# Performance work log

Measured on AMD Instinct MI355X. Metric: run time of the kernel, lower is better.

Reference implementation:

```python
import jax, jax.numpy as jnp
import numpy as np

W_DIM = 512
C_IN = 512
C_OUT = 512
K = 3
EPS = 1e-6
STYLE_SCALE = 1.0 / np.sqrt(W_DIM)              # EqualizedWeight scale for (out,in)
CONV_SCALE = 1.0 / np.sqrt(C_IN * K * K)        # EqualizedWeight scale for (out,in,k,k)


def setup_inputs() -> dict:
    key = jax.random.key(0)
    ks = jax.random.split(key, 6)
    B, H, W = 16, 64, 64
    return {
        "x": jax.random.normal(ks[0], (B, C_IN, H, W), dtype=jnp.float32),
        "w": jax.random.normal(ks[1], (B, W_DIM), dtype=jnp.float32),
        "style_weight": jax.random.normal(ks[2], (C_IN, W_DIM), dtype=jnp.float32),
        "style_bias": jnp.zeros((C_IN,), dtype=jnp.float32),
        "conv_weight": jax.random.normal(ks[3], (C_OUT, C_IN, K, K), dtype=jnp.float32),
        "noise_weight": jax.random.normal(ks[4], (1, C_OUT, 1, 1), dtype=jnp.float32),
        "bias": jnp.zeros((C_OUT,), dtype=jnp.float32),
        "noise": jax.random.normal(ks[5], (B, 1, H, W), dtype=jnp.float32),
    }


def reference(x, w, style_weight, style_bias, conv_weight, noise_weight, bias, noise):
    B, _, H, Wd = x.shape
    # to_style: equalized linear  [B, C_IN]
    s = w @ (style_weight * STYLE_SCALE).T + style_bias
    # modulate: [B, C_OUT, C_IN, K, K]
    wts = (conv_weight * CONV_SCALE)[None] * s[:, None, :, None, None]
    # demodulate
    sigma = jax.lax.rsqrt(jnp.sum(wts * wts, axis=(2, 3, 4)) + EPS)  # [B, C_OUT]
    wts = wts * sigma[:, :, None, None, None]
    # grouped conv with groups = batch
    x_r = x.reshape(1, B * C_IN, H, Wd)
    w_r = wts.reshape(B * C_OUT, C_IN, K, K)
    y = jax.lax.conv_general_dilated(
        x_r, w_r, window_strides=(1, 1), padding=[(1, 1), (1, 1)],
        dimension_numbers=("NCHW", "OIHW", "NCHW"), feature_group_count=B,
    ).reshape(B, C_OUT, H, Wd)
    # noise injection + bias + leaky relu(0.2)
    y = y + noise_weight * noise + bias[None, :, None, None]
    return jax.nn.leaky_relu(y, negative_slope=0.2)
```

## Files before the change

kernel.cpp:

```cpp
#include <hip/hip_runtime.h>


typedef __attribute__((ext_vector_type(8))) short short8;
typedef __attribute__((ext_vector_type(4))) float f32x4;

#define STYLE_SCALE 0.044194173824159216f
#define CONV_SCALE  0.014731391274719742f
#define CS2         (1.0f/4608.0f)

static __device__ __forceinline__ unsigned short f2bf(float x) {
    union { float f; unsigned int u; } a; a.f = x;
    unsigned int r = a.u + 0x7fffu + ((a.u >> 16) & 1u);
    return (unsigned short)(r >> 16);
}

static __device__ __forceinline__ void gl_lds16(const void* g, void* l) {
    __builtin_amdgcn_global_load_lds(
        (const __attribute__((address_space(1))) unsigned int*)g,
        (__attribute__((address_space(3))) unsigned int*)l, 16, 0, 0);
}

__global__ void k_style(const float* __restrict__ w, const float* __restrict__ sw,
                        const float* __restrict__ sb, float* __restrict__ s) {
    int b = blockIdx.y, j0 = blockIdx.x * 64, t = threadIdx.x;
    __shared__ float wl[512];
    __shared__ float part[256];
    wl[t] = w[b*512 + t]; wl[t+256] = w[b*512 + t + 256];
    __syncthreads();
    int jl = t & 63, seg = t >> 6;
    const float4* row = (const float4*)(sw + (size_t)(j0 + jl)*512) + seg*32;
    const float*  wv  = wl + seg*128;
    float acc = 0.f;
#pragma unroll 4
    for (int k = 0; k < 32; ++k) {
        float4 v = row[k];
        acc += v.x*wv[4*k] + v.y*wv[4*k+1] + v.z*wv[4*k+2] + v.w*wv[4*k+3];
    }
    part[t] = acc;
    __syncthreads();
    if (t < 64)
        s[b*512 + j0 + t] = (part[t] + part[t+64] + part[t+128] + part[t+192])
                            * STYLE_SCALE + sb[j0 + t];
}

__global__ void k_wprep(const float* __restrict__ cw, float* __restrict__ csq,
                        unsigned short* __restrict__ cwt) {
    int o = blockIdx.x, t = threadIdx.x;
    __shared__ float row[4608];
    const float4* src = (const float4*)(cw + (size_t)o*4608);
    for (int i = t; i < 1152; i += 256) ((float4*)row)[i] = src[i];
    __syncthreads();
#pragma unroll
    for (int it = 0; it < 2; ++it) {
        int i = t + it*256;
        float a = 0.f;
#pragma unroll
        for (int k = 0; k < 9; ++k) { float v = row[i*9 + k]; a += v*v; }
        csq[(size_t)o*512 + i] = a * CS2;
    }
    for (int p = t; p < 576; p += 256) {
        int ic = p / 36, rem = p % 36;
        int tap = rem >> 2, g = rem & 3;
        int i0 = ic*32 + g*8;
        union { unsigned short us[8]; uint4 q; } u;
#pragma unroll
        for (int j = 0; j < 8; ++j)
            u.us[j] = f2bf(row[(i0 + j)*9 + tap] * CONV_SCALE);
        size_t dst = (((size_t)(o >> 6)*16 + ic)*36 + rem)*64 + (o & 63);
        *(uint4*)(cwt + dst*8) = u.q;
    }
}

__global__ void k_sigma(const float* __restrict__ s, const float* __restrict__ csq,
                        float* __restrict__ sig) {
    int b = blockIdx.y, o0 = blockIdx.x * 64, t = threadIdx.x;
    __shared__ float s2l[512];
    __shared__ float part[256];
    float v0 = s[b*512 + t], v1 = s[b*512 + t + 256];
    s2l[t] = v0*v0; s2l[t+256] = v1*v1;
    __syncthreads();
    int ol = t & 63, seg = t >> 6;
    const float4* row = (const float4*)(csq + (size_t)(o0 + ol)*512) + seg*32;
    const float*  sv  = s2l + seg*128;
    float acc = 0.f;
#pragma unroll 4
    for (int k = 0; k < 32; ++k) {
        float4 c = row[k];
        acc += c.x*sv[4*k] + c.y*sv[4*k+1] + c.z*sv[4*k+2] + c.w*sv[4*k+3];
    }
    part[t] = acc;
    __syncthreads();
    if (t < 64)
        sig[b*512 + o0 + t] = 1.0f / sqrtf(part[t] + part[t+64] + part[t+128]
                                           + part[t+192] + 1e-6f);
}

__global__ void k_xt(const float* __restrict__ x, const float* __restrict__ s,
                     unsigned short* __restrict__ xt) {
    int h = blockIdx.x, b = blockIdx.y, t = threadIdx.x;
    __shared__ float tile[64][65];
    __shared__ float sl[64];
    for (int c0 = 0; c0 < 512; c0 += 64) {
        if (t < 64) sl[t] = s[b*512 + c0 + t];
#pragma unroll
        for (int it = 0; it < 4; ++it) {
            int idx = t + it*256;
            int c = idx >> 4, w4 = (idx & 15) * 4;
            float4 v = *(const float4*)(x + ((size_t)(b*512 + c0 + c)*4096) + h*64 + w4);
            tile[c][w4]   = v.x; tile[c][w4+1] = v.y;
            tile[c][w4+2] = v.z; tile[c][w4+3] = v.w;
        }
        __syncthreads();
#pragma unroll
        for (int it = 0; it < 2; ++it) {
            int idx = t + it*256;
            int wq = idx >> 3, c = (idx & 7) * 8;
            union { unsigned short us[8]; uint4 q; } u;
#pragma unroll
            for (int j = 0; j < 8; ++j)
                u.us[j] = f2bf(tile[c + j][wq] * sl[c + j]);
            *(uint4*)(xt + ((size_t)(b*4096 + h*64 + wq)*512 + c0 + c)) = u.q;
        }
        __syncthreads();
    }
}

__global__ __launch_bounds__(256, 3)
void k_conv(const unsigned short* __restrict__ xt, const unsigned short* __restrict__ cwt,
            const float* __restrict__ sig, const float* __restrict__ nw,
            const float* __restrict__ bias, const float* __restrict__ noise,
            float* __restrict__ out) {
    __shared__ __align__(16) short xs_s[2][6*64*32];

    const int tid  = threadIdx.x;
    const int lane = tid & 63;
    const int wave = tid >> 6;
    const int quad = lane >> 4;
    const int l15  = lane & 15;

    const int flat  = blockIdx.x;
    const int chunk = flat & 7, idx = flat >> 3;
    const int pxblk = idx & 15;
    const int oblk  = (idx >> 4) & 7;
    const int b     = chunk*2 + (idx >> 7);
    const int o0 = oblk * 64, h0 = pxblk * 4;

    if (h0 == 0)
        for (int i = tid; i < 1024; i += 256) {
            ((unsigned int*)xs_s[0])[i] = 0u;
            ((unsigned int*)xs_s[1])[i] = 0u;
        }
    if (h0 == 60)
        for (int i = tid; i < 1024; i += 256) {
            ((unsigned int*)xs_s[0])[5*1024 + i] = 0u;
            ((unsigned int*)xs_s[1])[5*1024 + i] = 0u;
        }

    const int pp = lane >> 2;
    const int cg = (lane & 3) ^ ((lane >> 3) & 3);

#define STAGE(bufidx, icn) do {                                              \
        short* dst_ = xs_s[bufidx];                                          \
        for (int q_ = wave; q_ < 24; q_ += 4) {                              \
            int r_ = q_ >> 2, p0_ = (q_ & 3) << 4;                           \
            int gr_ = h0 - 1 + r_;                                           \
            if (gr_ >= 0 && gr_ < 64)                                        \
                gl_lds16(xt + ((size_t)(b*4096 + gr_*64 + p0_ + pp)*512      \
                               + (icn)*32 + cg*8),                           \
                         dst_ + (r_*64 + p0_)*32);                           \
        } } while (0)

    f32x4 acc[4][4];
#pragma unroll
    for (int mt = 0; mt < 4; ++mt)
#pragma unroll
        for (int nt = 0; nt < 4; ++nt) acc[mt][nt] = (f32x4){0.f,0.f,0.f,0.f};

    const unsigned short* cwbase = cwt + (size_t)oblk*294912 + (size_t)quad*512
                                       + (size_t)l15*8;

    STAGE(0, 0);
    __syncthreads();

    const short8 z8 = {};

    for (int ic = 0; ic < 16; ++ic) {
        const unsigned short* cwA = cwbase + (size_t)ic*18432;
        const short8* xp = (const short8*)xs_s[ic & 1];
        if (ic < 15) STAGE((ic + 1) & 1, ic + 1);

#define LOADA(dst, tap) do { _Pragma("unroll")                               \
        for (int mt_ = 0; mt_ < 4; ++mt_)                                    \
            dst[mt_] = *(const short8*)(cwA + (tap)*2048 + mt_*128);         \
        } while (0)

#define TAP(AF, BF) do {                                                     \
        __builtin_amdgcn_s_setprio(1);                                       \
        _Pragma("unroll")                                                    \
        for (int mt_ = 0; mt_ < 4; ++mt_) { _Pragma("unroll")                \
            for (int nt_ = 0; nt_ < 4; ++nt_)                                \
                acc[mt_][nt_] = __builtin_amdgcn_mfma_f32_16x16x32_bf16(     \
                    AF[mt_], BF[nt_], acc[mt_][nt_], 0, 0, 0);               \
        }                                                                    \
        __builtin_amdgcn_s_setprio(0);                                       \
        } while (0)

#define LOADB(bf, d, dx, colS) do {                                          \
            const int base_ = (wave + (d))*256 + (colS);                     \
            if ((dx) == 0) {                                                 \
                int a0_ = (l15 == 0) ? base_ : base_ - 64;                   \
                bf[0] = xp[a0_];        bf[1] = xp[base_];                   \
                bf[2] = xp[base_ + 64]; bf[3] = xp[base_ + 128];             \
                if (l15 == 0) bf[0] = z8;                                    \
            } else if ((dx) == 1) {                                          \
                bf[0] = xp[base_ - 64]; bf[1] = xp[base_];                   \
                bf[2] = xp[base_ + 64]; bf[3] = xp[base_ + 128];             \
            } else {                                                         \
                int a3_ = (l15 == 15) ? base_ : base_ + 128;                 \
                bf[0] = xp[base_ - 64]; bf[1] = xp[base_];                   \
                bf[2] = xp[base_ + 64]; bf[3] = xp[a3_];                     \
            }                                                                \
        } while (0)

#define DXBODY(dx) do {                                                      \
            const int cs_   = l15 + (dx) + 15;                               \
            const int slot_ = quad ^ ((cs_ >> 1) & 3);                       \
            const int colS_ = cs_*4 + slot_;                                 \
            short8 af[4], ag[4], b0[4], b1[4];                               \
            LOADA(af, dx);                                 \
            LOADA(ag, (dx) + 3);                           \
            LOADB(b0, 0, dx, colS_);                                         \
            LOADB(b1, 1, dx, colS_);                                         \
            if ((dx) == 2 && l15 == 15) { b0[3] = z8; b1[3] = z8; }          \
            TAP(af, b0);                                                     \
            LOADA(af, (dx) + 6);                 \
            LOADB(b0, 2, dx, colS_);            \
            if ((dx) == 2 && l15 == 15) b0[3] = z8;                          \
            TAP(ag, b1);                                                     \
            TAP(af, b0);                                                     \
        } while (0)

        DXBODY(0);
        DXBODY(1);
        DXBODY(2);
#undef DXBODY
#undef LOADB
#undef TAP
#undef LOADA
        __syncthreads();
    }
#undef STAGE

    const int h = h0 + wave;
    float nz[4];
#pragma unroll
    for (int nt = 0; nt < 4; ++nt) nz[nt] = noise[b*4096 + h*64 + nt*16 + l15];
#pragma unroll
    for (int mt = 0; mt < 4; ++mt) {
#pragma unroll
        for (int r = 0; r < 4; ++r) {
            int o = o0 + mt*16 + quad*4 + r;
            float sg  = sig[b*512 + o];
            float nwv = nw[o], bv = bias[o];
#pragma unroll
            for (int nt = 0; nt < 4; ++nt) {
                float v = acc[mt][nt][r] * sg + nwv * nz[nt] + bv;
                v = (v >= 0.f) ? v : 0.2f * v;
                out[((size_t)(b*512 + o)*4096) + h*64 + nt*16 + l15] = v;
            }
        }
    }
}

extern "C" void kernel_launch(void* const* d_in, const int* in_sizes, int n_in,
                              void* d_out, int out_size, void* d_ws, size_t ws_size,
                              hipStream_t stream) {
    const float* x     = (const float*)d_in[0];
    const float* w     = (const float*)d_in[1];
    const float* sw    = (const float*)d_in[2];
    const float* sb    = (const float*)d_in[3];
    const float* cw    = (const float*)d_in[4];
    const float* nw    = (const float*)d_in[5];
    const float* bias  = (const float*)d_in[6];
    const float* noise = (const float*)d_in[7];
    float* out = (float*)d_out;

    char* ws = (char*)d_ws;
    unsigned short* xt  = (unsigned short*)(ws + 0);
    unsigned short* cwt = (unsigned short*)(ws + 67108864);
    float* s   = (float*)(ws + 71827456);
    float* sig = (float*)(ws + 71860224);
    float* csq = (float*)(ws + 71892992);

    k_wprep<<<512, 256, 0, stream>>>(cw, csq, cwt);
    k_style<<<dim3(8, 16), 256, 0, stream>>>(w, sw, sb, s);
    k_sigma<<<dim3(8, 16), 256, 0, stream>>>(s, csq, sig);
    k_xt   <<<dim3(64, 16), 256, 0, stream>>>(x, s, xt);
    k_conv <<<dim3(2048), 256, 0, stream>>>(xt, cwt, sig, nw, bias, noise, out);
}
```

Baseline: 500.6 us.

## Software-pipeline A/B fragment loads with ping-pong registers across taps

Restructures the inner 3x3 tap loop into a flat ping-pong schedule: A (weight) and B (LDS activation) fragments for the next tap load while the current tap's MFMAs run, and the first A fragment of the next input-channel chunk is prefetched before the barrier. Staging address computation is hoisted out of the loop into precomputed pointers and validity flags, and the s_setprio hints are removed. The aim is to hide global and LDS load latency behind MFMA work and cut per-iteration address arithmetic. The cost is higher register pressure, and removing setprio changes wave scheduling.

```diff
diff --git a/kernel.cpp b/kernel.cpp
--- a/kernel.cpp
+++ b/kernel.cpp
@@ -159,16 +159,21 @@
     const int pp = lane >> 2;
     const int cg = (lane & 3) ^ ((lane >> 3) & 3);
 
-#define STAGE(bufidx, icn) do {                                              \
-        short* dst_ = xs_s[bufidx];                                          \
-        for (int q_ = wave; q_ < 24; q_ += 4) {                              \
-            int r_ = q_ >> 2, p0_ = (q_ & 3) << 4;                           \
-            int gr_ = h0 - 1 + r_;                                           \
-            if (gr_ >= 0 && gr_ < 64)                                        \
-                gl_lds16(xt + ((size_t)(b*4096 + gr_*64 + p0_ + pp)*512      \
-                               + (icn)*32 + cg*8),                           \
-                         dst_ + (r_*64 + p0_)*32);                           \
-        } } while (0)
+    const unsigned short* sgp[6];
+    int  sdo[6];
+    bool sv [6];
+#pragma unroll
+    for (int k = 0; k < 6; ++k) {
+        int q = wave + 4*k, r = q >> 2, p0 = (q & 3) << 4;
+        int gr = h0 - 1 + r;
+        sv[k]  = (gr >= 0 && gr < 64);
+        sgp[k] = xt + ((size_t)(b*4096 + gr*64 + p0 + pp)*512 + cg*8);
+        sdo[k] = (r*64 + p0)*32;
+    }
+#define STAGE(bufidx, icn) do { _Pragma("unroll")                            \
+        for (int k_ = 0; k_ < 6; ++k_)                                       \
+            if (sv[k_]) gl_lds16(sgp[k_] + (icn)*32, xs_s[bufidx] + sdo[k_]);\
+        } while (0)
 
     f32x4 acc[4][4];
 #pragma unroll
@@ -176,79 +181,71 @@
 #pragma unroll
         for (int nt = 0; nt < 4; ++nt) acc[mt][nt] = (f32x4){0.f,0.f,0.f,0.f};
 
-    const unsigned short* cwbase = cwt + (size_t)oblk*294912 + (size_t)quad*512
-                                       + (size_t)l15*8;
+    const unsigned short* cwp = cwt + (size_t)oblk*294912 + (size_t)quad*512
+                                    + (size_t)l15*8;
+
+    const int wb  = wave * 256;
+    const int cs0 = l15 + 15, c0 = wb + cs0*4 + (quad ^ ((cs0 >> 1) & 3));
+    const int cs1 = l15 + 16, c1 = wb + cs1*4 + (quad ^ ((cs1 >> 1) & 3));
+    const int cs2 = l15 + 17, c2 = wb + cs2*4 + (quad ^ ((cs2 >> 1) & 3));
+    const bool e0 = (l15 == 0), e2 = (l15 == 15);
 
     STAGE(0, 0);
     __syncthreads();
 
+    short8 A0[4], A1[4], B0[4], B1[4];
     const short8 z8 = {};
 
-    for (int ic = 0; ic < 16; ++ic) {
-        const unsigned short* cwA = cwbase + (size_t)ic*18432;
-        const short8* xp = (const short8*)xs_s[ic & 1];
-        if (ic < 15) STAGE((ic + 1) & 1, ic + 1);
-
-#define LOADA(dst, tap) do { _Pragma("unroll")                               \
+#define LDA(dst, ptr, tap) { _Pragma("unroll")                               \
         for (int mt_ = 0; mt_ < 4; ++mt_)                                    \
-            dst[mt_] = *(const short8*)(cwA + (tap)*2048 + mt_*128);         \
-        } while (0)
-
-#define TAP(AF, BF) do {                                                     \
-        __builtin_amdgcn_s_setprio(1);                                       \
-        _Pragma("unroll")                                                    \
+            dst[mt_] = *(const short8*)((ptr) + (tap)*2048 + mt_*128); }
+
+#define LDB0(dst, d) { const int b_ = c0 + (d)*256;                          \
+        int a0_ = e0 ? b_ : b_ - 64;                                         \
+        dst[0] = xp[a0_];      dst[1] = xp[b_];                              \
+        dst[2] = xp[b_ + 64];  dst[3] = xp[b_ + 128];                        \
+        if (e0) dst[0] = z8; }
+#define LDB1(dst, d) { const int b_ = c1 + (d)*256;                          \
+        dst[0] = xp[b_ - 64];  dst[1] = xp[b_];                              \
+        dst[2] = xp[b_ + 64];  dst[3] = xp[b_ + 128]; }
+#define LDB2(dst, d) { const int b_ = c2 + (d)*256;                          \
+        int a3_ = e2 ? b_ : b_ + 128;                                        \
+        dst[0] = xp[b_ - 64];  dst[1] = xp[b_];                              \
+        dst[2] = xp[b_ + 64];  dst[3] = xp[a3_];                             \
+        if (e2) dst[3] = z8; }
+
+#define TAP(AF, BF) { _Pragma("unroll")                                      \
         for (int mt_ = 0; mt_ < 4; ++mt_) { _Pragma("unroll")                \
             for (int nt_ = 0; nt_ < 4; ++nt_)                                \
                 acc[mt_][nt_] = __builtin_amdgcn_mfma_f32_16x16x32_bf16(     \
-                    AF[mt_], BF[nt_], acc[mt_][nt_], 0, 0, 0);               \
-        }                                                                    \
-        __builtin_amdgcn_s_setprio(0);                                       \
-        } while (0)
-
-#define LOADB(bf, d, dx, colS) do {                                          \
-            const int base_ = (wave + (d))*256 + (colS);                     \
-            if ((dx) == 0) {                                                 \
-                int a0_ = (l15 == 0) ? base_ : base_ - 64;                   \
-                bf[0] = xp[a0_];        bf[1] = xp[base_];                   \
-                bf[2] = xp[base_ + 64]; bf[3] = xp[base_ + 128];             \
-                if (l15 == 0) bf[0] = z8;                                    \
-            } else if ((dx) == 1) {                                          \
-                bf[0] = xp[base_ - 64]; bf[1] = xp[base_];                   \
-                bf[2] = xp[base_ + 64]; bf[3] = xp[base_ + 128];             \
-            } else {                                                         \
-                int a3_ = (l15 == 15) ? base_ : base_ + 128;                 \
-                bf[0] = xp[base_ - 64]; bf[1] = xp[base_];                   \
-                bf[2] = xp[base_ + 64]; bf[3] = xp[a3_];                     \
-            }                                                                \
-        } while (0)
-
-#define DXBODY(dx) do {                                                      \
-            const int cs_   = l15 + (dx) + 15;                               \
-            const int slot_ = quad ^ ((cs_ >> 1) & 3);                       \
-            const int colS_ = cs_*4 + slot_;                                 \
-            short8 af[4], ag[4], b0[4], b1[4];                               \
-            LOADA(af, dx);                                 \
-            LOADA(ag, (dx) + 3);                           \
-            LOADB(b0, 0, dx, colS_);                                         \
-            LOADB(b1, 1, dx, colS_);                                         \
-            if ((dx) == 2 && l15 == 15) { b0[3] = z8; b1[3] = z8; }          \
-            TAP(af, b0);                                                     \
-            LOADA(af, (dx) + 6);                 \
-            LOADB(b0, 2, dx, colS_);            \
-            if ((dx) == 2 && l15 == 15) b0[3] = z8;                          \
-            TAP(ag, b1);                                                     \
-            TAP(af, b0);                                                     \
-        } while (0)
-
-        DXBODY(0);
-        DXBODY(1);
-        DXBODY(2);
-#undef DXBODY
-#undef LOADB
+                    AF[mt_], BF[nt_], acc[mt_][nt_], 0, 0, 0); } }
+
+    LDA(A0, cwp, 0);
+
+    for (int ic = 0; ic < 16; ++ic) {
+        const short8* xp = (const short8*)xs_s[ic & 1];
+        if (ic < 15) STAGE((ic + 1) & 1, ic + 1);
+        const unsigned short* cwn = (ic < 15) ? cwp + 18432 : cwp;
+
+        LDB0(B0, 0);
+        LDA(A1, cwp, 3);  LDB0(B1, 1);  TAP(A0, B0);
+        LDA(A0, cwp, 6);  LDB0(B0, 2);  TAP(A1, B1);
+        LDA(A1, cwp, 1);  LDB1(B1, 0);  TAP(A0, B0);
+        LDA(A0, cwp, 4);  LDB1(B0, 1);  TAP(A1, B1);
+        LDA(A1, cwp, 7);  LDB1(B1, 2);  TAP(A0, B0);
+        LDA(A0, cwp, 2);  LDB2(B0, 0);  TAP(A1, B1);
+        LDA(A1, cwp, 5);  LDB2(B1, 1);  TAP(A0, B0);
+        LDA(A0, cwp, 8);  LDB2(B0, 2);  TAP(A1, B1);
+        TAP(A0, B0);
+        LDA(A0, cwn, 0);
+        cwp = cwn;
+        __syncthreads();
+    }
 #undef TAP
-#undef LOADA
-        __syncthreads();
-    }
+#undef LDB0
+#undef LDB1
+#undef LDB2
+#undef LDA
 #undef STAGE
 
     const int h = h0 + wave;
```

After: 543.9 us. 8.6% more time.
